# Kernel tuning notes

Measured on AMD Instinct MI355X. Metric: run time of the kernel, lower is better.

Reference implementation:

```python
import jax, jax.numpy as jnp
import numpy as np

B, G, N, D = 8, 16, 256, 768
E, S, SEQ = 1536, 128, 512
EPS = 1e-05


def rope_gn(x):
    # x: [b, g, n, h, s]; positions run over flattened (g, n), matching rope(x, dim=[1,2])
    g, n, half = x.shape[1], x.shape[2], x.shape[-1] // 2
    position = jnp.arange(g * n, dtype=jnp.float32).reshape(g, n)[:, :, None]  # [g,n,1]
    inv_freq = 10000.0 ** (jnp.arange(half, dtype=jnp.float32) / half)
    sinusoid = position[..., None] * inv_freq  # [g,n,1,half]
    sin, cos = jnp.sin(sinusoid), jnp.cos(sinusoid)
    x1, x2 = jnp.split(x, 2, axis=-1)
    return jnp.concatenate([x1 * cos - x2 * sin, x2 * cos + x1 * sin], axis=-1)


def rel_pos_bias(w, seq_len):
    # Toeplitz construction (seq_len <= 512 branch). w: [2*seq_len-1] -> [1, seq_len, seq_len]
    t = jnp.pad(w, (0, seq_len))                  # [3*seq_len-1]
    t = jnp.tile(t, seq_len)[:-seq_len]           # [seq_len*(3*seq_len-2)]
    t = t.reshape(seq_len, 3 * seq_len - 2)
    r = seq_len - 1                                # (2*seq_len-1)//2
    return t[:, r:-r][None]                        # [1, seq_len, seq_len]


def setup_inputs():
    key = jax.random.key(0)
    ks = jax.random.split(key, 8)
    inputs = jax.random.normal(ks[0], (B, G, N, D), dtype=jnp.float32)
    seg = jax.random.randint(ks[1], (B, G * N), 0, 4)
    segment_ids = jnp.sort(seg, axis=-1).reshape(B, G, N)
    params = {
        'ln_w': jnp.ones((D,), jnp.float32),
        'ln_b': jnp.zeros((D,), jnp.float32),
        'W1': jax.random.normal(ks[2], (D, 2 * E + S), jnp.float32) * 0.02,
        'b1': jnp.zeros((2 * E + S,), jnp.float32),
        'gamma': jax.random.uniform(ks[3], (4, S), jnp.float32),
        'beta': jax.random.uniform(ks[4], (4, S), jnp.float32),
        'W2': jax.random.normal(ks[5], (E, D), jnp.float32) * 0.02,
        'b2': jnp.zeros((D,), jnp.float32),
        'w_rel': jax.random.uniform(ks[6], (2 * SEQ - 1,), jnp.float32),
    }
    return dict(inputs=inputs, segment_ids=segment_ids, **params)


def reference(inputs, segment_ids, ln_w, ln_b, W1, b1, gamma, beta, W2, b2, w_rel):
    b, g, n, d = inputs.shape
    shortcut = inputs
    # LayerNorm
    mu = inputs.mean(-1, keepdims=True)
    var = ((inputs - mu) ** 2).mean(-1, keepdims=True)
    x = (inputs - mu) * jax.lax.rsqrt(var + EPS) * ln_w + ln_b
    # dense1 + silu, split into u, v, z
    uv = jax.nn.silu(x @ W1 + b1)
    u, v, z = uv[..., :E], uv[..., E:2 * E], uv[..., 2 * E:]
    # per-head affine gating + rope
    z = z[..., None, :] * gamma + beta            # [b,g,n,4,s]
    z = rope_gn(z)
    quad_q, quad_k, lin_q, lin_k = (z[..., i, :] for i in range(4))
    # non-causal global linear attention
    kv = jnp.einsum('bgcs,bgce->bse', lin_k, v)
    lin_v = jnp.einsum('bgcs,bse->bgce', lin_q, kv)
    lin_kv = jnp.einsum('bgnk,bgne->bgke', lin_k, lin_v) / n
    # segment mask over chunks
    mn = segment_ids.min(-1)
    mx = segment_ids.max(-1)
    mask = ((mn[:, :, None] <= mx[:, None, :]) & (mx[:, :, None] >= mn[:, None, :])).astype(inputs.dtype)
    mask = mask / mask.sum(-1, keepdims=True)
    lin_kv = jnp.einsum('bhke,bgh->bgke', lin_kv, mask)
    linear = jnp.einsum('bgnk,bgke->bgne', lin_q, lin_kv)
    # quadratic relu^2 attention with relative position bias
    qk = jnp.einsum('bgnk,bgmk->bgnm', quad_q, quad_k)
    bias = rel_pos_bias(w_rel, SEQ)[:, :n, :n]    # [1,n,n] broadcasts to [b,g,n,n]
    kernel = jnp.square(jax.nn.relu(qk / n + bias))
    quadratic = jnp.einsum('bgnm,bgme->bgne', kernel, v)
    out = (u * (quadratic + linear)) @ W2 + b2 + shortcut
    return out
```

## Files before the change

kernel.cpp:

```cpp
#include <hip/hip_runtime.h>
#include <math.h>

typedef __bf16 bf16;
typedef __bf16 bf16x8 __attribute__((ext_vector_type(8)));
typedef __bf16 bf16x4 __attribute__((ext_vector_type(4)));
typedef float  f32x4  __attribute__((ext_vector_type(4)));

#define D_   768
#define E_   1536
#define S_   128
#define TT_  32768
#define B_   8

#define OFF_W1T   0UL
#define OFF_W2T   4915200UL
#define OFF_TAB   7274496UL
#define OFF_XN    9375744UL
#define OFF_KER   OFF_XN
#define OFF_QQ    (OFF_XN + 16777216UL)
#define OFF_QK    (OFF_XN + 25165824UL)
#define OFF_LQ    (OFF_XN + 33554432UL)
#define OFF_U     59707392UL
#define OFF_Z     160370688UL
#define OFF_LK    168759296UL
#define OFF_LQT   177147904UL
#define OFF_LKT   185536512UL
#define OFF_MASK  193925120UL
#define OFF_INVF  193933312UL

__device__ __forceinline__ void gl_lds16(const bf16* g, bf16* l) {
  __builtin_amdgcn_global_load_lds(
      (const __attribute__((address_space(1))) unsigned int*)g,
      (__attribute__((address_space(3))) unsigned int*)l, 16, 0, 0);
}

#define BM 128
#define BN 128
#define BK 32

template <class Epi, bool DUAL, bool SWZ = false>
__global__ __launch_bounds__(256) void gemm_bt(
    const bf16* __restrict__ A, const bf16* __restrict__ B,
    int lda, int ldb, int K,
    long sAb, long sAg, long sBb, long sBg,
    const bf16* __restrict__ A2, const bf16* __restrict__ B2,
    int lda2, int ldb2, int K2,
    long sA2b, long sA2g, long sB2b, long sB2g,
    int gdiv, Epi epi)
{
  __shared__ bf16 As[BM * BK];
  __shared__ bf16 Bs[BN * BK];
  const int z = blockIdx.z;
  const int bb = z / gdiv, gg = z % gdiv;

  int bx = blockIdx.x, by = blockIdx.y;
  if constexpr (SWZ) {
    const int nbx = gridDim.x, nby = gridDim.y, nwg = nbx * nby;
    int bid = by * nbx + bx;
    const int q = nwg >> 3, r = nwg & 7;
    const int xcd = bid & 7, lid = bid >> 3;
    bid = (xcd < r ? xcd * (q + 1) : r * (q + 1) + (xcd - r) * q) + lid;
    const int gm = 8;
    const int pig = gm * nby;
    const int grp = bid / pig;
    const int fm = grp * gm;
    const int szm = min(nbx - fm, gm);
    const int loc = bid - grp * pig;
    bx = fm + loc % szm;
    by = loc / szm;
  }

  const int tid  = threadIdx.x;
  const int lane = tid & 63, wave = tid >> 6;
  const int wm = (wave >> 1) * 64, wn = (wave & 1) * 64;
  const int lrow = lane & 15, quad = lane >> 4;
  const int srow = wave * 16 + (lane >> 2);
  const int scol = (lane & 3) * 8;
  bf16* ldsA0 = As + wave * 512;
  bf16* ldsA1 = As + (wave + 4) * 512;
  bf16* ldsB0 = Bs + wave * 512;
  bf16* ldsB1 = Bs + (wave + 4) * 512;

  f32x4 acc[4][4] = {};

  auto kloop = [&](const bf16* __restrict__ Ab, const bf16* __restrict__ Bb,
                   int lda_, int ldb_, int K_) {
    for (int k0 = 0; k0 < K_; k0 += BK) {
      __syncthreads();
      gl_lds16(Ab + (long)srow * lda_ + k0 + scol,        ldsA0);
      gl_lds16(Ab + (long)(srow + 64) * lda_ + k0 + scol, ldsA1);
      gl_lds16(Bb + (long)srow * ldb_ + k0 + scol,        ldsB0);
      gl_lds16(Bb + (long)(srow + 64) * ldb_ + k0 + scol, ldsB1);
      __syncthreads();
      bf16x8 af[4], bfr[4];
#pragma unroll
      for (int i = 0; i < 4; i++) af[i]  = *(const bf16x8*)&As[(wm + i * 16 + lrow) * BK + quad * 8];
#pragma unroll
      for (int i = 0; i < 4; i++) bfr[i] = *(const bf16x8*)&Bs[(wn + i * 16 + lrow) * BK + quad * 8];
#pragma unroll
      for (int mi = 0; mi < 4; mi++)
#pragma unroll
        for (int ni = 0; ni < 4; ni++)
          acc[mi][ni] = __builtin_amdgcn_mfma_f32_16x16x32_bf16(af[mi], bfr[ni], acc[mi][ni], 0, 0, 0);
    }
  };

  kloop(A + (long)bb * sAb + (long)gg * sAg + (long)bx * BM * lda,
        B + (long)bb * sBb + (long)gg * sBg + (long)by * BN * ldb, lda, ldb, K);
  if constexpr (DUAL)
    kloop(A2 + (long)bb * sA2b + (long)gg * sA2g + (long)bx * BM * lda2,
          B2 + (long)bb * sB2b + (long)gg * sB2g + (long)by * BN * ldb2, lda2, ldb2, K2);

  const int rowbase = bx * BM + wm + quad * 4;
  const int colbase = by * BN + wn + lrow;
#pragma unroll
  for (int mi = 0; mi < 4; mi++)
#pragma unroll
    for (int ni = 0; ni < 4; ni++)
      epi(rowbase + mi * 16, colbase + ni * 16, bb, gg, acc[mi][ni]);
}

struct EpiGemm1 {
  const float* b1; bf16* u; bf16* vT; bf16* z;
  __device__ void operator()(int row0, int col, int, int, f32x4 a) const {
    float s[4];
    const float bias = b1[col];
#pragma unroll
    for (int j = 0; j < 4; j++) {
      float x = a[j] + bias;
      float e = __expf(-x);
      s[j] = __fdividef(x, 1.f + e);
    }
    if (col < E_) {
#pragma unroll
      for (int j = 0; j < 4; j++) u[(long)(row0 + j) * E_ + col] = (bf16)s[j];
    } else if (col < 2 * E_) {
      const int e = col - E_, b = row0 >> 12, t = row0 & 4095;
      bf16x4 o;
#pragma unroll
      for (int j = 0; j < 4; j++) o[j] = (bf16)s[j];
      *(bf16x4*)&vT[((long)(b * E_ + e)) * 4096 + t] = o;
    } else {
      const int sc = col - 2 * E_;
#pragma unroll
      for (int j = 0; j < 4; j++) z[(long)(row0 + j) * S_ + sc] = (bf16)s[j];
    }
  }
};
struct EpiF32 {
  float* C; long sCb, sCg; int ldc;
  __device__ void operator()(int row0, int col, int bb, int gg, f32x4 a) const {
#pragma unroll
    for (int j = 0; j < 4; j++)
      C[(long)bb * sCb + (long)gg * sCg + (long)(row0 + j) * ldc + col] = a[j];
  }
};
struct EpiBf16 {
  bf16* C; long sCb, sCg; int ldc;
  __device__ void operator()(int row0, int col, int bb, int gg, f32x4 a) const {
#pragma unroll
    for (int j = 0; j < 4; j++)
      C[(long)bb * sCb + (long)gg * sCg + (long)(row0 + j) * ldc + col] = (bf16)a[j];
  }
};
struct EpiKer {
  bf16* C; const float* wrel;
  __device__ void operator()(int row0, int col, int bb, int, f32x4 a) const {
#pragma unroll
    for (int j = 0; j < 4; j++) {
      float v = a[j] * (1.f / 256.f) + wrel[511 + col - (row0 + j)];
      v = fmaxf(v, 0.f);
      C[(long)bb * 65536 + (long)(row0 + j) * 256 + col] = (bf16)(v * v);
    }
  }
};
struct EpiCombine {
  bf16* u;
  __device__ void operator()(int row0, int col, int bb, int gg, f32x4 a) const {
#pragma unroll
    for (int j = 0; j < 4; j++) {
      long idx = ((long)((bb * 16 + gg) * 256 + row0 + j)) * E_ + col;
      u[idx] = (bf16)((float)u[idx] * a[j]);
    }
  }
};
struct EpiFinal {
  float* out; const float* b2; const float* x0;
  __device__ void operator()(int row0, int col, int, int, f32x4 a) const {
#pragma unroll
    for (int j = 0; j < 4; j++) {
      long idx = (long)(row0 + j) * D_ + col;
      out[idx] = a[j] + b2[col] + x0[idx];
    }
  }
};

__global__ __launch_bounds__(256) void ln_kernel(
    const float* __restrict__ x, const float* __restrict__ w,
    const float* __restrict__ b, bf16* __restrict__ xn)
{
  const long t = blockIdx.x;
  const float* row = x + t * D_;
  const int tid = threadIdx.x;
  float v0 = row[tid], v1 = row[tid + 256], v2 = row[tid + 512];
  float s = v0 + v1 + v2;
  float sq = v0 * v0 + v1 * v1 + v2 * v2;
#pragma unroll
  for (int off = 32; off; off >>= 1) {
    s  += __shfl_down(s, off, 64);
    sq += __shfl_down(sq, off, 64);
  }
  __shared__ float red[2][4];
  const int wave = tid >> 6, lane = tid & 63;
  if (lane == 0) { red[0][wave] = s; red[1][wave] = sq; }
  __syncthreads();
  s  = red[0][0] + red[0][1] + red[0][2] + red[0][3];
  sq = red[1][0] + red[1][1] + red[1][2] + red[1][3];
  const float mean = s * (1.f / 768.f);
  const float var  = sq * (1.f / 768.f) - mean * mean;
  const float rs   = rsqrtf(var + 1e-5f);
  xn[t * D_ + tid]       = (bf16)((v0 - mean) * rs * w[tid] + b[tid]);
  xn[t * D_ + tid + 256] = (bf16)((v1 - mean) * rs * w[tid + 256] + b[tid + 256]);
  xn[t * D_ + tid + 512] = (bf16)((v2 - mean) * rs * w[tid + 512] + b[tid + 512]);
}

template <class TI>
__global__ __launch_bounds__(256) void transpose_cast(
    const TI* __restrict__ in, bf16* __restrict__ out,
    int R, int C, long sInB, long sOutB)
{
  __shared__ float tile[64][65];
  const TI* ib = in  + (long)blockIdx.z * sInB;
  bf16*     ob = out + (long)blockIdx.z * sOutB;
  const int c0 = blockIdx.x * 64, r0 = blockIdx.y * 64;
  const int lc = threadIdx.x & 63, lr0 = threadIdx.x >> 6;
#pragma unroll
  for (int i = 0; i < 16; i++) {
    int r = lr0 + i * 4;
    tile[r][lc] = (float)ib[(long)(r0 + r) * C + c0 + lc];
  }
  __syncthreads();
#pragma unroll
  for (int i = 0; i < 16; i++) {
    int r = lr0 + i * 4;
    ob[(long)(c0 + r) * R + r0 + lc] = (bf16)tile[lc][r];
  }
}

__global__ __launch_bounds__(256) void rope_table_kernel(
    const float* __restrict__ invf, float2* __restrict__ tab)
{
  int idx = blockIdx.x * 256 + threadIdx.x;
  int p = idx >> 6, i = idx & 63;
  float arg = (float)p * invf[i];
  double a = (double)arg;
  tab[idx] = make_float2((float)sin(a), (float)cos(a));
}

__global__ __launch_bounds__(128) void rope_kernel(
    const bf16* __restrict__ zbuf, const float* __restrict__ gamma,
    const float* __restrict__ beta, const float2* __restrict__ tab,
    bf16* __restrict__ qq, bf16* __restrict__ qk,
    bf16* __restrict__ lq, bf16* __restrict__ lk)
{
  const long t = blockIdx.x;
  const int s = threadIdx.x;
  const int p = (int)(t & 4095);
  const int i = s & 63;
  const float2 sc = tab[p * 64 + i];
  const bf16* zr = zbuf + t * S_;
  const float zlo = (float)zr[i], zhi = (float)zr[i + 64];
  bf16* outs[4] = {qq, qk, lq, lk};
#pragma unroll
  for (int r = 0; r < 4; r++) {
    float zl = zlo * gamma[r * 128 + i]      + beta[r * 128 + i];
    float zh = zhi * gamma[r * 128 + i + 64] + beta[r * 128 + i + 64];
    float val = (s < 64) ? (zl * sc.y - zh * sc.x) : (zh * sc.y + zl * sc.x);
    outs[r][t * S_ + s] = (bf16)val;
  }
}

__global__ __launch_bounds__(64) void mask_kernel(const int* __restrict__ seg, float* __restrict__ mask) {
  __shared__ int mn[16], mx[16];
  const int b = blockIdx.x, tid = threadIdx.x;
  if (tid < 16) {
    const int* p = seg + (long)b * 4096 + tid * 256;
    int lo = p[0], hi = p[0];
    for (int i = 1; i < 256; i++) { int v = p[i]; lo = min(lo, v); hi = max(hi, v); }
    mn[tid] = lo; mx[tid] = hi;
  }
  __syncthreads();
  if (tid < 16) {
    const int g = tid;
    float row[16]; float s = 0.f;
    for (int h = 0; h < 16; h++) {
      float o = (mn[g] <= mx[h] && mx[g] >= mn[h]) ? 1.f : 0.f;
      row[h] = o; s += o;
    }
    const float inv = 1.f / s;
    for (int h = 0; h < 16; h++) mask[((long)b * 16 + g) * 16 + h] = row[h] * inv;
  }
}

__global__ __launch_bounds__(256) void mix_kernel(
    const float* __restrict__ P2, const float* __restrict__ mask, bf16* __restrict__ amix)
{
  const int z = blockIdx.x;
  const int b = z >> 4;
  float m[16];
#pragma unroll
  for (int h = 0; h < 16; h++) m[h] = mask[(long)z * 16 + h] * (1.f / 256.f);
  const float* Pb = P2 + (long)b * 16 * 16384;
  bf16* Ab = amix + (long)z * 16384;
#pragma unroll 4
  for (int j = 0; j < 16; j++) {
    int c = j * 256 + threadIdx.x;
    float ax = 0, ay = 0, az = 0, aw = 0;
#pragma unroll
    for (int h = 0; h < 16; h++) {
      float4 p = ((const float4*)(Pb + (long)h * 16384))[c];
      ax += m[h] * p.x; ay += m[h] * p.y; az += m[h] * p.z; aw += m[h] * p.w;
    }
    bf16x4 o; o[0] = (bf16)ax; o[1] = (bf16)ay; o[2] = (bf16)az; o[3] = (bf16)aw;
    *(bf16x4*)&Ab[(long)c * 4] = o;
  }
}

extern "C" void kernel_launch(void* const* d_in, const int* in_sizes, int n_in,
                              void* d_out, int out_size, void* d_ws, size_t ws_size,
                              hipStream_t stream)
{
  const float* x0    = (const float*)d_in[0];
  const int*   seg   = (const int*)d_in[1];
  const float* lnw   = (const float*)d_in[2];
  const float* lnb   = (const float*)d_in[3];
  const float* W1    = (const float*)d_in[4];
  const float* b1    = (const float*)d_in[5];
  const float* gamma = (const float*)d_in[6];
  const float* beta  = (const float*)d_in[7];
  const float* W2    = (const float*)d_in[8];
  const float* b2    = (const float*)d_in[9];
  const float* wrel  = (const float*)d_in[10];
  float* out = (float*)d_out;
  char* ws = (char*)d_ws;

  bf16*   w1t   = (bf16*)(ws + OFF_W1T);
  bf16*   w2t   = (bf16*)(ws + OFF_W2T);
  float2* tab   = (float2*)(ws + OFF_TAB);
  bf16*   xn    = (bf16*)(ws + OFF_XN);
  bf16*   ker   = (bf16*)(ws + OFF_KER);
  bf16*   qq    = (bf16*)(ws + OFF_QQ);
  bf16*   qk    = (bf16*)(ws + OFF_QK);
  bf16*   lq    = (bf16*)(ws + OFF_LQ);
  bf16*   u     = (bf16*)(ws + OFF_U);
  bf16*   zb    = (bf16*)(ws + OFF_Z);
  float*  P2    = (float*)(ws + OFF_Z);
  bf16*   lk    = (bf16*)(ws + OFF_LK);
  bf16*   T1    = (bf16*)(ws + OFF_LK);
  bf16*   lqT   = (bf16*)(ws + OFF_LQT);
  bf16*   amix  = (bf16*)(ws + OFF_LQT);
  bf16*   kvT   = (bf16*)(ws + OFF_LQT + 4194304UL);
  bf16*   lkT   = (bf16*)(ws + OFF_LKT);
  float*  maskb = (float*)(ws + OFF_MASK);
  float*  invfd = (float*)(ws + OFF_INVF);
  bf16*   vTd   = (bf16*)d_out;

  static float h_invf[64];
  for (int i = 0; i < 64; i++) h_invf[i] = powf(10000.0f, (float)i * (1.0f / 64.0f));
  hipMemcpyAsync(invfd, h_invf, 64 * sizeof(float), hipMemcpyHostToDevice, stream);

  transpose_cast<float><<<dim3(50, 12, 1), 256, 0, stream>>>(W1, w1t, 768, 3200, 0, 0);
  transpose_cast<float><<<dim3(12, 24, 1), 256, 0, stream>>>(W2, w2t, 1536, 768, 0, 0);
  rope_table_kernel<<<1024, 256, 0, stream>>>(invfd, tab);
  mask_kernel<<<8, 64, 0, stream>>>(seg, maskb);

  ln_kernel<<<TT_, 256, 0, stream>>>(x0, lnw, lnb, xn);

  gemm_bt<EpiGemm1, false, true><<<dim3(256, 25, 1), 256, 0, stream>>>(
      xn, w1t, 768, 768, 768, 0, 0, 0, 0,
      nullptr, nullptr, 0, 0, 0, 0, 0, 0, 0, 1, EpiGemm1{b1, u, vTd, zb});

  rope_kernel<<<TT_, 128, 0, stream>>>(zb, gamma, beta, tab, qq, qk, lq, lk);

  transpose_cast<bf16><<<dim3(2, 64, 8), 256, 0, stream>>>(lq, lqT, 4096, 128, 524288, 524288);
  transpose_cast<bf16><<<dim3(2, 64, 8), 256, 0, stream>>>(lk, lkT, 4096, 128, 524288, 524288);

  gemm_bt<EpiF32, false><<<dim3(1, 1, 128), 256, 0, stream>>>(
      lqT, lkT, 4096, 4096, 256, 524288, 256, 524288, 256,
      nullptr, nullptr, 0, 0, 0, 0, 0, 0, 0, 16, EpiF32{P2, 262144, 16384, 128});

  mix_kernel<<<128, 256, 0, stream>>>(P2, maskb, amix);

  gemm_bt<EpiBf16, false><<<dim3(12, 1, 8), 256, 0, stream>>>(
      vTd, lkT, 4096, 4096, 4096, 6291456, 0, 524288, 0,
      nullptr, nullptr, 0, 0, 0, 0, 0, 0, 0, 1, EpiBf16{kvT, 196608, 0, 128});

  gemm_bt<EpiBf16, false><<<dim3(2, 1, 128), 256, 0, stream>>>(
      lq, amix, 128, 128, 128, 32768, 0, 16384, 0,
      nullptr, nullptr, 0, 0, 0, 0, 0, 0, 0, 1, EpiBf16{T1, 32768, 0, 128});

  gemm_bt<EpiKer, false><<<dim3(2, 2, 128), 256, 0, stream>>>(
      qq, qk, 128, 128, 128, 32768, 0, 32768, 0,
      nullptr, nullptr, 0, 0, 0, 0, 0, 0, 0, 1, EpiKer{ker, wrel});

  gemm_bt<EpiCombine, true><<<dim3(2, 12, 128), 256, 0, stream>>>(
      ker, vTd, 256, 4096, 256, 1048576, 65536, 6291456, 256,
      T1, kvT, 128, 128, 128, 524288, 32768, 196608, 0, 16, EpiCombine{u});

  gemm_bt<EpiFinal, false, true><<<dim3(256, 6, 1), 256, 0, stream>>>(
      u, w2t, 1536, 1536, 1536, 0, 0, 0, 0,
      nullptr, nullptr, 0, 0, 0, 0, 0, 0, 0, 1, EpiFinal{out, b2, x0});
}
```

Baseline: 1.038 ms.

## Add 256x256 eight-wave pipelined GEMM for the two large projections

```diff
diff --git a/kernel.cpp b/kernel.cpp
--- a/kernel.cpp
+++ b/kernel.cpp
@@ -34,24 +34,20 @@
       (__attribute__((address_space(3))) unsigned int*)l, 16, 0, 0);
 }
 
-#define BM 128
-#define BN 128
-#define BK 32
-
-template <class Epi, bool DUAL, bool SWZ = false>
-__global__ __launch_bounds__(256) void gemm_bt(
+
+#define STG(GB, LD, KT, DSTH) do {                                        \
+  const int cg_ = (lane & 7) ^ ((lane >> 3) & 7);                         \
+  const int rg_ = wave * 16 + ((lane >> 3) << 1) + (cg_ >> 2);            \
+  gl_lds16((GB) + (long)rg_ * (LD) + (KT) * 32 + (cg_ & 3) * 8,           \
+           (DSTH) + wave * 512);                                          \
+} while (0)
+
+template <class Epi, bool SWZ>
+__global__ __launch_bounds__(512, 2) void gemm8p(
     const bf16* __restrict__ A, const bf16* __restrict__ B,
-    int lda, int ldb, int K,
-    long sAb, long sAg, long sBb, long sBg,
-    const bf16* __restrict__ A2, const bf16* __restrict__ B2,
-    int lda2, int ldb2, int K2,
-    long sA2b, long sA2g, long sB2b, long sB2g,
-    int gdiv, Epi epi)
-{
-  __shared__ bf16 As[BM * BK];
-  __shared__ bf16 Bs[BN * BK];
-  const int z = blockIdx.z;
-  const int bb = z / gdiv, gg = z % gdiv;
+    int lda, int ldb, int K, Epi epi)
+{
+  __shared__ bf16 smem[4][4][4096];
 
   int bx = blockIdx.x, by = blockIdx.y;
   if constexpr (SWZ) {
@@ -72,6 +68,129 @@
 
   const int tid  = threadIdx.x;
   const int lane = tid & 63, wave = tid >> 6;
+  const int wr = wave >> 2, wc = wave & 3;
+  const int lrow = lane & 15, quad = lane >> 4;
+  const int rb16 = (wc & 1) * 4;
+  const int lbase = (lrow >> 1) * 128 +
+                    (((((lrow & 1) << 2) | quad) ^ ((lrow >> 1) & 7)) * 16);
+
+  const bf16* gA0 = A + (long)(bx * 256)       * lda;
+  const bf16* gA1 = A + (long)(bx * 256 + 128) * lda;
+  const bf16* gB0 = B + (long)(by * 256)       * ldb;
+  const bf16* gB1 = B + (long)(by * 256 + 128) * ldb;
+
+  f32x4 acc[8][4] = {};
+  bf16x8 afr[4], bfrag[4];
+
+  const int NT = K >> 5;
+
+#pragma unroll
+  for (int t = 0; t < 3; ++t) {
+    STG(gA0, lda, t, &smem[t][0][0]);
+    STG(gA1, lda, t, &smem[t][1][0]);
+    STG(gB0, ldb, t, &smem[t][2][0]);
+    STG(gB1, ldb, t, &smem[t][3][0]);
+  }
+  asm volatile("s_waitcnt vmcnt(8)" ::: "memory");
+  __builtin_amdgcn_s_barrier();
+
+  for (int t = 0; t < NT; ++t) {
+    const int st = t & 3, sp = (t + 3) & 3;
+    const bf16* aBuf = &smem[st][wr][0];
+    const bf16* bBuf = &smem[st][2 + (wc >> 1)][0];
+    const bool stg = (t + 3 < NT);
+
+#pragma unroll
+    for (int mi = 0; mi < 4; ++mi)
+      afr[mi] = *(const bf16x8*)((const char*)aBuf + mi * 1024 + lbase);
+#pragma unroll
+    for (int k = 0; k < 4; ++k)
+      bfrag[k] = *(const bf16x8*)((const char*)bBuf + (rb16 + k) * 1024 + lbase);
+    if (stg) { STG(gA0, lda, t + 3, &smem[sp][0][0]);
+               STG(gB0, ldb, t + 3, &smem[sp][2][0]); }
+    __builtin_amdgcn_sched_barrier(0);
+    __builtin_amdgcn_s_barrier();
+    __builtin_amdgcn_s_setprio(1);
+#pragma unroll
+    for (int mi = 0; mi < 4; ++mi)
+#pragma unroll
+      for (int n4 = 0; n4 < 4; ++n4)
+        acc[mi][n4] = __builtin_amdgcn_mfma_f32_16x16x32_bf16(
+            afr[mi], bfrag[n4], acc[mi][n4], 0, 0, 0);
+    __builtin_amdgcn_s_setprio(0);
+    __builtin_amdgcn_sched_barrier(0);
+    __builtin_amdgcn_s_barrier();
+
+#pragma unroll
+    for (int mi = 0; mi < 4; ++mi)
+      afr[mi] = *(const bf16x8*)((const char*)aBuf + (4 + mi) * 1024 + lbase);
+    if (stg) { STG(gA1, lda, t + 3, &smem[sp][1][0]);
+               STG(gB1, ldb, t + 3, &smem[sp][3][0]); }
+    __builtin_amdgcn_sched_barrier(0);
+    __builtin_amdgcn_s_barrier();
+    __builtin_amdgcn_s_setprio(1);
+#pragma unroll
+    for (int mi = 0; mi < 4; ++mi)
+#pragma unroll
+      for (int n4 = 0; n4 < 4; ++n4)
+        acc[4 + mi][n4] = __builtin_amdgcn_mfma_f32_16x16x32_bf16(
+            afr[mi], bfrag[n4], acc[4 + mi][n4], 0, 0, 0);
+    __builtin_amdgcn_s_setprio(0);
+    __builtin_amdgcn_sched_barrier(0);
+
+    if (t + 3 < NT)      asm volatile("s_waitcnt vmcnt(8)" ::: "memory");
+    else if (t + 2 < NT) asm volatile("s_waitcnt vmcnt(4)" ::: "memory");
+    else if (t + 1 < NT) asm volatile("s_waitcnt vmcnt(0)" ::: "memory");
+    if (t + 1 < NT) __builtin_amdgcn_s_barrier();
+  }
+
+  const int rowbase = bx * 256 + wr * 128 + quad * 4;
+  const int colbase = by * 256 + wc * 64 + lrow;
+#pragma unroll
+  for (int mi = 0; mi < 8; mi++)
+#pragma unroll
+    for (int ni = 0; ni < 4; ni++)
+      epi(rowbase + mi * 16, colbase + ni * 16, 0, 0, acc[mi][ni]);
+}
+
+#define BM 128
+#define BN 128
+#define BK 32
+
+template <class Epi, bool DUAL, bool SWZ = false>
+__global__ __launch_bounds__(256) void gemm_bt(
+    const bf16* __restrict__ A, const bf16* __restrict__ B,
+    int lda, int ldb, int K,
+    long sAb, long sAg, long sBb, long sBg,
+    const bf16* __restrict__ A2, const bf16* __restrict__ B2,
+    int lda2, int ldb2, int K2,
+    long sA2b, long sA2g, long sB2b, long sB2g,
+    int gdiv, Epi epi)
+{
+  __shared__ bf16 As[BM * BK];
+  __shared__ bf16 Bs[BN * BK];
+  const int z = blockIdx.z;
+  const int bb = z / gdiv, gg = z % gdiv;
+
+  int bx = blockIdx.x, by = blockIdx.y;
+  if constexpr (SWZ) {
+    const int nbx = gridDim.x, nby = gridDim.y, nwg = nbx * nby;
+    int bid = by * nbx + bx;
+    const int q = nwg >> 3, r = nwg & 7;
+    const int xcd = bid & 7, lid = bid >> 3;
+    bid = (xcd < r ? xcd * (q + 1) : r * (q + 1) + (xcd - r) * q) + lid;
+    const int gm = 8;
+    const int pig = gm * nby;
+    const int grp = bid / pig;
+    const int fm = grp * gm;
+    const int szm = min(nbx - fm, gm);
+    const int loc = bid - grp * pig;
+    bx = fm + loc % szm;
+    by = loc / szm;
+  }
+
+  const int tid  = threadIdx.x;
+  const int lane = tid & 63, wave = tid >> 6;
   const int wm = (wave >> 1) * 64, wn = (wave & 1) * 64;
   const int lrow = lane & 15, quad = lane >> 4;
   const int srow = wave * 16 + (lane >> 2);
@@ -144,6 +263,18 @@
       const int sc = col - 2 * E_;
 #pragma unroll
       for (int j = 0; j < 4; j++) z[(long)(row0 + j) * S_ + sc] = (bf16)s[j];
+    }
+  }
+};
+struct EpiZ {
+  const float* b1; bf16* z;
+  __device__ void operator()(int row0, int col, int, int, f32x4 a) const {
+    const float bias = b1[2 * E_ + col];
+#pragma unroll
+    for (int j = 0; j < 4; j++) {
+      float x = a[j] + bias;
+      float e = __expf(-x);
+      z[(long)(row0 + j) * S_ + col] = (bf16)__fdividef(x, 1.f + e);
     }
   }
 };
@@ -376,9 +507,11 @@
 
   ln_kernel<<<TT_, 256, 0, stream>>>(x0, lnw, lnb, xn);
 
-  gemm_bt<EpiGemm1, false, true><<<dim3(256, 25, 1), 256, 0, stream>>>(
-      xn, w1t, 768, 768, 768, 0, 0, 0, 0,
-      nullptr, nullptr, 0, 0, 0, 0, 0, 0, 0, 1, EpiGemm1{b1, u, vTd, zb});
+  gemm8p<EpiGemm1, true><<<dim3(128, 12), 512, 0, stream>>>(
+      xn, w1t, 768, 768, 768, EpiGemm1{b1, u, vTd, zb});
+  gemm_bt<EpiZ, false><<<dim3(256, 1, 1), 256, 0, stream>>>(
+      xn, w1t + (long)3072 * 768, 768, 768, 768, 0, 0, 0, 0,
+      nullptr, nullptr, 0, 0, 0, 0, 0, 0, 0, 1, EpiZ{b1, zb});
 
   rope_kernel<<<TT_, 128, 0, stream>>>(zb, gamma, beta, tab, qq, qk, lq, lk);
 
@@ -407,7 +540,6 @@
       ker, vTd, 256, 4096, 256, 1048576, 65536, 6291456, 256,
       T1, kvT, 128, 128, 128, 524288, 32768, 196608, 0, 16, EpiCombine{u});
 
-  gemm_bt<EpiFinal, false, true><<<dim3(256, 6, 1), 256, 0, stream>>>(
-      u, w2t, 1536, 1536, 1536, 0, 0, 0, 0,
-      nullptr, nullptr, 0, 0, 0, 0, 0, 0, 0, 1, EpiFinal{out, b2, x0});
-}
+  gemm8p<EpiFinal, true><<<dim3(128, 3), 512, 0, stream>>>(
+      u, w2t, 1536, 1536, 1536, EpiFinal{out, b2, x0});
+}
```

Result: faster. 989.2 us (-4.7%).

## Triple-buffer GEMM with swizzled LDS and split-K the kv reduction

Applied to the files above, without the earlier changes.

```diff
diff --git a/kernel.cpp b/kernel.cpp
--- a/kernel.cpp
+++ b/kernel.cpp
@@ -34,12 +34,18 @@
       (__attribute__((address_space(3))) unsigned int*)l, 16, 0, 0);
 }
 
-#define BM 128
-#define BN 128
-#define BK 32
-
-template <class Epi, bool DUAL, bool SWZ = false>
-__global__ __launch_bounds__(256) void gemm_bt(
+
+#define STG2(GB, LD, KT, DSTH) do {                                       \
+  const int cg_ = (lane & 7) ^ ((lane >> 3) & 7);                         \
+  const int rg_ = wave * 32 + ((lane >> 3) << 1) + (cg_ >> 2);            \
+  gl_lds16((GB) + (long)rg_ * (LD) + (KT) * 32 + (cg_ & 3) * 8,           \
+           (DSTH) + wave * 1024);                                         \
+  gl_lds16((GB) + (long)(rg_ + 16) * (LD) + (KT) * 32 + (cg_ & 3) * 8,    \
+           (DSTH) + wave * 1024 + 512);                                   \
+} while (0)
+
+template <class Epi, bool DUAL, bool SWZ>
+__global__ __launch_bounds__(256, 3) void gemm3s(
     const bf16* __restrict__ A, const bf16* __restrict__ B,
     int lda, int ldb, int K,
     long sAb, long sAg, long sBb, long sBg,
@@ -48,8 +54,8 @@
     long sA2b, long sA2g, long sB2b, long sB2g,
     int gdiv, Epi epi)
 {
-  __shared__ bf16 As[BM * BK];
-  __shared__ bf16 Bs[BN * BK];
+  __shared__ bf16 smem[3][2][4096];
+
   const int z = blockIdx.z;
   const int bb = z / gdiv, gg = z % gdiv;
 
@@ -72,47 +78,71 @@
 
   const int tid  = threadIdx.x;
   const int lane = tid & 63, wave = tid >> 6;
-  const int wm = (wave >> 1) * 64, wn = (wave & 1) * 64;
+  const int wr = wave >> 1, wc = wave & 1;
   const int lrow = lane & 15, quad = lane >> 4;
-  const int srow = wave * 16 + (lane >> 2);
-  const int scol = (lane & 3) * 8;
-  bf16* ldsA0 = As + wave * 512;
-  bf16* ldsA1 = As + (wave + 4) * 512;
-  bf16* ldsB0 = Bs + wave * 512;
-  bf16* ldsB1 = Bs + (wave + 4) * 512;
+  const int lbase = (lrow >> 1) * 128 +
+                    (((((lrow & 1) << 2) | quad) ^ ((lrow >> 1) & 7)) * 16);
 
   f32x4 acc[4][4] = {};
-
-  auto kloop = [&](const bf16* __restrict__ Ab, const bf16* __restrict__ Bb,
-                   int lda_, int ldb_, int K_) {
-    for (int k0 = 0; k0 < K_; k0 += BK) {
-      __syncthreads();
-      gl_lds16(Ab + (long)srow * lda_ + k0 + scol,        ldsA0);
-      gl_lds16(Ab + (long)(srow + 64) * lda_ + k0 + scol, ldsA1);
-      gl_lds16(Bb + (long)srow * ldb_ + k0 + scol,        ldsB0);
-      gl_lds16(Bb + (long)(srow + 64) * ldb_ + k0 + scol, ldsB1);
-      __syncthreads();
-      bf16x8 af[4], bfr[4];
-#pragma unroll
-      for (int i = 0; i < 4; i++) af[i]  = *(const bf16x8*)&As[(wm + i * 16 + lrow) * BK + quad * 8];
-#pragma unroll
-      for (int i = 0; i < 4; i++) bfr[i] = *(const bf16x8*)&Bs[(wn + i * 16 + lrow) * BK + quad * 8];
-#pragma unroll
-      for (int mi = 0; mi < 4; mi++)
-#pragma unroll
-        for (int ni = 0; ni < 4; ni++)
-          acc[mi][ni] = __builtin_amdgcn_mfma_f32_16x16x32_bf16(af[mi], bfr[ni], acc[mi][ni], 0, 0, 0);
+  bf16x8 af[4], bf_[4];
+
+  auto run = [&](const bf16* __restrict__ gA, const bf16* __restrict__ gB,
+                 int lda_, int ldb_, int K_, bool first) {
+    const int NT = K_ >> 5;
+    if (!first) __syncthreads();
+    STG2(gA, lda_, 0, &smem[0][0][0]);
+    STG2(gB, ldb_, 0, &smem[0][1][0]);
+    STG2(gA, lda_, 1, &smem[1][0][0]);
+    STG2(gB, ldb_, 1, &smem[1][1][0]);
+    asm volatile("s_waitcnt vmcnt(4)" ::: "memory");
+    __builtin_amdgcn_s_barrier();
+    __builtin_amdgcn_sched_barrier(0);
+
+    int st = 0, sp = 2;
+    for (int t = 0; t < NT; ++t) {
+      const bf16* aBuf = &smem[st][0][0];
+      const bf16* bBuf = &smem[st][1][0];
+
+#pragma unroll
+      for (int mi = 0; mi < 4; ++mi)
+        af[mi] = *(const bf16x8*)((const char*)aBuf + (wr * 4 + mi) * 1024 + lbase);
+#pragma unroll
+      for (int ni = 0; ni < 4; ++ni)
+        bf_[ni] = *(const bf16x8*)((const char*)bBuf + (wc * 4 + ni) * 1024 + lbase);
+      if (t + 2 < NT) {
+        STG2(gA, lda_, t + 2, &smem[sp][0][0]);
+        STG2(gB, ldb_, t + 2, &smem[sp][1][0]);
+      }
+
+      __builtin_amdgcn_s_setprio(1);
+#pragma unroll
+      for (int mi = 0; mi < 4; ++mi)
+#pragma unroll
+        for (int ni = 0; ni < 4; ++ni)
+          acc[mi][ni] = __builtin_amdgcn_mfma_f32_16x16x32_bf16(
+              af[mi], bf_[ni], acc[mi][ni], 0, 0, 0);
+      __builtin_amdgcn_s_setprio(0);
+
+      __builtin_amdgcn_sched_barrier(0);
+      if (t + 2 < NT)      asm volatile("s_waitcnt vmcnt(4)" ::: "memory");
+      else if (t + 1 < NT) asm volatile("s_waitcnt vmcnt(0)" ::: "memory");
+      if (t + 1 < NT) {
+        __builtin_amdgcn_s_barrier();
+        __builtin_amdgcn_sched_barrier(0);
+      }
+      st = (st == 2) ? 0 : st + 1;
+      sp = (sp == 2) ? 0 : sp + 1;
     }
   };
 
-  kloop(A + (long)bb * sAb + (long)gg * sAg + (long)bx * BM * lda,
-        B + (long)bb * sBb + (long)gg * sBg + (long)by * BN * ldb, lda, ldb, K);
+  run(A + bb * sAb + gg * sAg + (long)bx * 128 * lda,
+      B + bb * sBb + gg * sBg + (long)by * 128 * ldb, lda, ldb, K, true);
   if constexpr (DUAL)
-    kloop(A2 + (long)bb * sA2b + (long)gg * sA2g + (long)bx * BM * lda2,
-          B2 + (long)bb * sB2b + (long)gg * sB2g + (long)by * BN * ldb2, lda2, ldb2, K2);
-
-  const int rowbase = bx * BM + wm + quad * 4;
-  const int colbase = by * BN + wn + lrow;
+    run(A2 + bb * sA2b + gg * sA2g + (long)bx * 128 * lda2,
+        B2 + bb * sB2b + gg * sB2g + (long)by * 128 * ldb2, lda2, ldb2, K2, false);
+
+  const int rowbase = bx * 128 + wr * 64 + quad * 4;
+  const int colbase = by * 128 + wc * 64 + lrow;
 #pragma unroll
   for (int mi = 0; mi < 4; mi++)
 #pragma unroll
@@ -194,6 +224,17 @@
     }
   }
 };
+
+__global__ __launch_bounds__(256) void kvsum_kernel(
+    const bf16* __restrict__ kv4, bf16* __restrict__ kvT)
+{
+  const long i = (long)blockIdx.x * 256 + threadIdx.x;
+  const int s = (int)(i & 127);
+  const long esb = i >> 7;
+  const bf16* p = kv4 + (esb << 9) + s;
+  float v = (float)p[0] + (float)p[128] + (float)p[256] + (float)p[384];
+  kvT[i] = (bf16)v;
+}
 
 __global__ __launch_bounds__(256) void ln_kernel(
     const float* __restrict__ x, const float* __restrict__ w,
@@ -351,6 +392,7 @@
   bf16*   ker   = (bf16*)(ws + OFF_KER);
   bf16*   qq    = (bf16*)(ws + OFF_QQ);
   bf16*   qk    = (bf16*)(ws + OFF_QK);
+  bf16*   kv4   = (bf16*)(ws + OFF_QQ);
   bf16*   lq    = (bf16*)(ws + OFF_LQ);
   bf16*   u     = (bf16*)(ws + OFF_U);
   bf16*   zb    = (bf16*)(ws + OFF_Z);
@@ -376,7 +418,7 @@
 
   ln_kernel<<<TT_, 256, 0, stream>>>(x0, lnw, lnb, xn);
 
-  gemm_bt<EpiGemm1, false, true><<<dim3(256, 25, 1), 256, 0, stream>>>(
+  gemm3s<EpiGemm1, false, true><<<dim3(256, 25, 1), 256, 0, stream>>>(
       xn, w1t, 768, 768, 768, 0, 0, 0, 0,
       nullptr, nullptr, 0, 0, 0, 0, 0, 0, 0, 1, EpiGemm1{b1, u, vTd, zb});
 
@@ -385,29 +427,30 @@
   transpose_cast<bf16><<<dim3(2, 64, 8), 256, 0, stream>>>(lq, lqT, 4096, 128, 524288, 524288);
   transpose_cast<bf16><<<dim3(2, 64, 8), 256, 0, stream>>>(lk, lkT, 4096, 128, 524288, 524288);
 
-  gemm_bt<EpiF32, false><<<dim3(1, 1, 128), 256, 0, stream>>>(
+  gemm3s<EpiF32, false, false><<<dim3(1, 1, 128), 256, 0, stream>>>(
       lqT, lkT, 4096, 4096, 256, 524288, 256, 524288, 256,
       nullptr, nullptr, 0, 0, 0, 0, 0, 0, 0, 16, EpiF32{P2, 262144, 16384, 128});
 
   mix_kernel<<<128, 256, 0, stream>>>(P2, maskb, amix);
 
-  gemm_bt<EpiBf16, false><<<dim3(12, 1, 8), 256, 0, stream>>>(
-      vTd, lkT, 4096, 4096, 4096, 6291456, 0, 524288, 0,
-      nullptr, nullptr, 0, 0, 0, 0, 0, 0, 0, 1, EpiBf16{kvT, 196608, 0, 128});
-
-  gemm_bt<EpiBf16, false><<<dim3(2, 1, 128), 256, 0, stream>>>(
+  gemm3s<EpiKer, false, false><<<dim3(2, 2, 128), 256, 0, stream>>>(
+      qq, qk, 128, 128, 128, 32768, 0, 32768, 0,
+      nullptr, nullptr, 0, 0, 0, 0, 0, 0, 0, 1, EpiKer{ker, wrel});
+
+  gemm3s<EpiBf16, false, false><<<dim3(12, 1, 32), 256, 0, stream>>>(
+      vTd, lkT, 4096, 4096, 1024, 6291456, 1024, 524288, 1024,
+      nullptr, nullptr, 0, 0, 0, 0, 0, 0, 0, 4, EpiBf16{kv4, 786432, 128, 512});
+  kvsum_kernel<<<6144, 256, 0, stream>>>(kv4, kvT);
+
+  gemm3s<EpiBf16, false, false><<<dim3(2, 1, 128), 256, 0, stream>>>(
       lq, amix, 128, 128, 128, 32768, 0, 16384, 0,
       nullptr, nullptr, 0, 0, 0, 0, 0, 0, 0, 1, EpiBf16{T1, 32768, 0, 128});
 
-  gemm_bt<EpiKer, false><<<dim3(2, 2, 128), 256, 0, stream>>>(
-      qq, qk, 128, 128, 128, 32768, 0, 32768, 0,
-      nullptr, nullptr, 0, 0, 0, 0, 0, 0, 0, 1, EpiKer{ker, wrel});
-
-  gemm_bt<EpiCombine, true><<<dim3(2, 12, 128), 256, 0, stream>>>(
+  gemm3s<EpiCombine, true, false><<<dim3(2, 12, 128), 256, 0, stream>>>(
       ker, vTd, 256, 4096, 256, 1048576, 65536, 6291456, 256,
       T1, kvT, 128, 128, 128, 524288, 32768, 196608, 0, 16, EpiCombine{u});
 
-  gemm_bt<EpiFinal, false, true><<<dim3(256, 6, 1), 256, 0, stream>>>(
+  gemm3s<EpiFinal, false, true><<<dim3(256, 6, 1), 256, 0, stream>>>(
       u, w2t, 1536, 1536, 1536, 0, 0, 0, 0,
       nullptr, nullptr, 0, 0, 0, 0, 0, 0, 0, 1, EpiFinal{out, b2, x0});
 }
```

Measured after the change: 858.5 us. 1.21x faster.
